# Kernel optimization log

Measured on AMD Instinct MI355X. Metric: run time of the kernel, lower is better.

Reference implementation:

```python
import jax, jax.numpy as jnp
import numpy as np

B, S, HID = 2, 2048, 4096
H, P, N, G, K = 128, 64, 128, 8, 4      # heads, head_dim, ssm_state, groups, conv kernel
INTER = H * P                           # 8192
CONV_DIM = INTER + 2 * G * N            # 10240
CHUNK = 128
EPS = 1e-5
DT_MIN, DT_MAX = 0.0, 100.0


def setup_inputs() -> dict:
    key = jax.random.key(0)
    ks = jax.random.split(key, 4)
    proj = INTER + CONV_DIM + H
    return {
        "x": jax.random.normal(ks[0], (B, S, HID), jnp.float32),
        "in_proj_w": jax.random.normal(ks[1], (proj, HID), jnp.float32) * 0.02,
        "conv_w": jax.random.normal(ks[2], (CONV_DIM, 1, K), jnp.float32) * 0.2,
        "conv_b": jnp.zeros((CONV_DIM,), jnp.float32),
        "dt_bias": jnp.ones((H,), jnp.float32),
        "A_log": jnp.log(jnp.arange(1, H + 1, dtype=jnp.float32)),
        "D": jnp.ones((H,), jnp.float32),
        "norm_w": jnp.ones((INTER,), jnp.float32),
        "out_proj_w": jax.random.normal(ks[3], (HID, INTER), jnp.float32) * 0.02,
    }


def _segsum(a):
    # a: (..., c) -> (..., c, c); [i, j] = sum_{k=j+1..i} a[k] for i >= j, else -inf
    c = a.shape[-1]
    s = jnp.cumsum(a, axis=-1)
    diff = s[..., :, None] - s[..., None, :]
    mask = jnp.tril(jnp.ones((c, c), dtype=bool))
    return jnp.where(mask, diff, -jnp.inf)


def reference(x, in_proj_w, conv_w, conv_b, dt_bias, A_log, D, norm_w, out_proj_w):
    b, s, _ = x.shape
    proj = jnp.einsum('bsd,ed->bse', x, in_proj_w)
    gate = proj[..., :INTER]
    hBC = proj[..., INTER:INTER + CONV_DIM]
    dt = proj[..., INTER + CONV_DIM:]                       # (b, s, H)

    # depthwise causal conv1d + silu
    xc = jnp.transpose(hBC, (0, 2, 1))                      # (b, conv_dim, s)
    xc = jax.lax.conv_general_dilated(xc, conv_w, (1,), [(K - 1, 0)],
                                      dimension_numbers=('NCH', 'OIH', 'NCH'),
                                      feature_group_count=CONV_DIM)
    xc = xc + conv_b[None, :, None]
    hBC = jax.nn.silu(jnp.transpose(xc, (0, 2, 1)))

    hs = hBC[..., :INTER].reshape(b, s, H, P)
    Bm = hBC[..., INTER:INTER + G * N].reshape(b, s, G, N)
    Cm = hBC[..., INTER + G * N:].reshape(b, s, G, N)

    A = -jnp.exp(A_log)                                     # (H,)
    dt = jnp.clip(jax.nn.softplus(dt + dt_bias), DT_MIN, DT_MAX)

    rep = H // G
    Bh = jnp.repeat(Bm, rep, axis=2)                        # (b, s, H, N)
    Ch = jnp.repeat(Cm, rep, axis=2)

    nc = s // CHUNK
    xch = (hs * dt[..., None]).reshape(b, nc, CHUNK, H, P)  # dt-scaled input, chunked
    Bc = Bh.reshape(b, nc, CHUNK, H, N)
    Cc = Ch.reshape(b, nc, CHUNK, H, N)
    A_dt = (dt * A).reshape(b, nc, CHUNK, H).transpose(0, 3, 1, 2)  # (b, H, nc, c)
    A_cum = jnp.cumsum(A_dt, axis=-1)

    # intra-chunk (diagonal) contribution
    L = jnp.exp(_segsum(A_dt))                              # (b, H, nc, c, c)
    Y_diag = jnp.einsum('bzlhn,bzshn,bhzls,bzshp->bzlhp', Cc, Bc, L, xch)

    # per-chunk final states
    decay_states = jnp.exp(A_cum[..., -1:] - A_cum)         # (b, H, nc, c)
    states = jnp.einsum('bzlhn,bhzl,bzlhp->bzhpn', Bc, decay_states, xch)

    # inter-chunk recurrence (initial state = 0)
    states_p = jnp.concatenate([jnp.zeros_like(states[:, :1]), states], axis=1)  # (b, nc+1, H, P, N)
    A_last = jnp.pad(A_cum[..., -1], ((0, 0), (0, 0), (1, 0)))                   # (b, H, nc+1)
    decay_chunk = jnp.exp(_segsum(A_last))                                        # (b, H, nc+1, nc+1)
    new_states = jnp.einsum('bhzc,bchpn->bzhpn', decay_chunk, states_p)
    prev = new_states[:, :-1]                                # state entering each chunk

    Y_off = jnp.einsum('bzlhn,bzhpn,bhzl->bzlhp', Cc, prev, jnp.exp(A_cum))
    Y = (Y_diag + Y_off).reshape(b, s, H, P) + hs * D[None, None, :, None]
    y = Y.reshape(b, s, INTER)

    # gated grouped RMSNorm (norm_before_gate=False)
    g = y * jax.nn.silu(gate)
    gg = g.reshape(b, s, G, INTER // G)
    var = jnp.mean(gg * gg, axis=-1, keepdims=True)
    gg = gg * jax.lax.rsqrt(var + EPS)
    out = gg.reshape(b, s, INTER) * norm_w

    return jnp.einsum('bsi,oi->bso', out, out_proj_w)
```

## Files before the change

### kernel.cpp

```cpp
#include <hip/hip_runtime.h>
#include <hip/hip_bf16.h>
#include <cstdint>
#include <cstddef>

#define DEVI __device__ __forceinline__

#define BB 2
#define S_LEN 2048
#define HID_DIM 4096
#define NH 128
#define PD 64
#define NS 128
#define NG 8
#define INTER 8192
#define CONVD 10240
#define PROJ 18560
#define PROJP 18688
#define NC 16
#define BS 4096
#define GN 1024

using short8 = __attribute__((ext_vector_type(8))) short;
using short4v = __attribute__((ext_vector_type(4))) short;
using f32x4  = __attribute__((ext_vector_type(4))) float;
using bf16x8 = __attribute__((ext_vector_type(8))) __bf16;

DEVI float bf2f(short u) {
  union { unsigned int i; float f; } v;
  v.i = ((unsigned int)(unsigned short)u) << 16;
  return v.f;
}
DEVI short f2bf(float f) {
  union { float ff; unsigned int i; } v; v.ff = f;
  unsigned int x = v.i;
  return (short)((x + 0x7fffu + ((x >> 16) & 1u)) >> 16);
}
DEVI f32x4 mfma16(short8 a, short8 b, f32x4 c) {
  return __builtin_amdgcn_mfma_f32_16x16x32_bf16(
      __builtin_bit_cast(bf16x8, a), __builtin_bit_cast(bf16x8, b), c, 0, 0, 0);
}
DEVI void gl_lds16(const short* g, short* l) {
  __builtin_amdgcn_global_load_lds(
      (const __attribute__((address_space(1))) void*)g,
      (__attribute__((address_space(3))) void*)l, 16, 0, 0);
}
DEVI float sigmoidf_(float x) { return 1.f / (1.f + __expf(-x)); }

__global__ __launch_bounds__(256) void cvt_f32_bf16_k(const float* __restrict__ in,
                                                      short* __restrict__ out, size_t n) {
  size_t i = ((size_t)blockIdx.x * 256 + threadIdx.x) * 8;
  if (i + 8 > n) return;
  float4 a = *(const float4*)(in + i);
  float4 b = *(const float4*)(in + i + 4);
  short8 o;
  o[0] = f2bf(a.x); o[1] = f2bf(a.y); o[2] = f2bf(a.z); o[3] = f2bf(a.w);
  o[4] = f2bf(b.x); o[5] = f2bf(b.y); o[6] = f2bf(b.z); o[7] = f2bf(b.w);
  *(short8*)(out + i) = o;
}


#define STG(ISB, BUF, KH, TILE) do { \
  const short* _src = (ISB) ? Bt : A; \
  const int _r0 = (ISB) ? n0 : m0; \
  short* _lb = lds_ + ((ISB) ? 32768 : 0) + ((BUF)*2+(KH))*8192; \
  const int _kt = (TILE)*64 + (KH)*32; \
  { int _row = (wid*2)*16 + srow; int _sl = sps ^ ((_row>>1)&3); \
    gl_lds16(_src + (size_t)(_r0+_row)*K + _kt + _sl*8, _lb + (wid*2)*512); } \
  { int _row = (wid*2+1)*16 + srow; int _sl = sps ^ ((_row>>1)&3); \
    gl_lds16(_src + (size_t)(_r0+_row)*K + _kt + _sl*8, _lb + (wid*2+1)*512); } \
} while(0)

#define NOPS ((void)0)
#define VM6 asm volatile("s_waitcnt vmcnt(6)" ::: "memory")
#define VM0 asm volatile("s_waitcnt vmcnt(0)" ::: "memory")

#define PH(BUF, KH, MIH, DOB, STGS, VMW) do { \
  _Pragma("unroll") \
  for (int _m = 0; _m < 4; ++_m) { \
    int _row = wr*128 + ((MIH)*4+_m)*16 + fr; \
    af[_m] = *(const short8*)(lds_ + ((BUF)*2+(KH))*8192 + _row*32 + ((slot ^ ((_row>>1)&3))<<3)); \
  } \
  if (DOB) { \
    _Pragma("unroll") \
    for (int _n = 0; _n < 4; ++_n) { \
      int _row = wc*64 + _n*16 + fr; \
      bf_[_n] = *(const short8*)(lds_ + 32768 + ((BUF)*2+(KH))*8192 + _row*32 + ((slot ^ ((_row>>1)&3))<<3)); \
    } \
  } \
  STGS; VMW; \
  __builtin_amdgcn_s_barrier(); \
  asm volatile("s_waitcnt lgkmcnt(0)" ::: "memory"); \
  __builtin_amdgcn_sched_barrier(0); \
  __builtin_amdgcn_s_setprio(1); \
  _Pragma("unroll") \
  for (int _m = 0; _m < 4; ++_m) \
    _Pragma("unroll") \
    for (int _n = 0; _n < 4; ++_n) \
      acc[(MIH)*4+_m][_n] = mfma16(af[_m], bf_[_n], acc[(MIH)*4+_m][_n]); \
  __builtin_amdgcn_s_setprio(0); \
  __builtin_amdgcn_s_barrier(); \
} while(0)

template<int CB16>
__global__ __launch_bounds__(512, 2) void gemm256_k(const short* __restrict__ A,
                                                    const short* __restrict__ Bt,
                                                    void* __restrict__ Cout,
                                                    int Nstride, int K, int ntn) {
  __shared__ short lds_[65536];
  const int tid = threadIdx.x, wid = tid >> 6, lane = tid & 63;
  const int nwg = gridDim.x, orig = blockIdx.x;
  const int swz = (orig & 7) * (nwg >> 3) + (orig >> 3);
  const int per_group = ntn << 4;
  const int group = swz / per_group;
  const int rem = swz - group * per_group;
  const int m0 = (group * 16 + (rem & 15)) * 256;
  const int n0 = (rem >> 4) * 256;
  const int wr = wid >> 2, wc = wid & 3;
  const int fr = lane & 15, slot = lane >> 4;
  const int srow = lane >> 2, sps = lane & 3;

  f32x4 acc[8][4] = {};
  short8 af[4], bf_[4];
  const int NT = K >> 6;

  STG(1, 0, 0, 0); STG(0, 0, 0, 0); STG(1, 0, 1, 0); STG(0, 0, 1, 0);
  asm volatile("s_waitcnt vmcnt(4)" ::: "memory");
  STG(1, 1, 0, 1); STG(0, 1, 0, 1); STG(1, 1, 1, 1);
  asm volatile("s_waitcnt vmcnt(6)" ::: "memory");
  __builtin_amdgcn_s_barrier();

  for (int i = 0; i < (NT >> 1) - 1; ++i) {
    const int t = 2 * i;
    PH(0, 0, 0, 1, STG(0, 1, 1, t + 1), NOPS);
    PH(0, 0, 1, 0, STG(1, 0, 0, t + 2), NOPS);
    PH(0, 1, 0, 1, STG(0, 0, 0, t + 2), NOPS);
    PH(0, 1, 1, 0, STG(1, 0, 1, t + 2), VM6);
    PH(1, 0, 0, 1, STG(0, 0, 1, t + 2), NOPS);
    PH(1, 0, 1, 0, STG(1, 1, 0, t + 3), NOPS);
    PH(1, 1, 0, 1, STG(0, 1, 0, t + 3), NOPS);
    PH(1, 1, 1, 0, STG(1, 1, 1, t + 3), VM6);
  }
  PH(0, 0, 0, 1, STG(0, 1, 1, NT - 1), NOPS);
  PH(0, 0, 1, 0, NOPS, NOPS);
  PH(0, 1, 0, 1, NOPS, NOPS);
  PH(0, 1, 1, 0, NOPS, VM0);
  PH(1, 0, 0, 1, NOPS, NOPS);
  PH(1, 0, 1, 0, NOPS, NOPS);
  PH(1, 1, 0, 1, NOPS, NOPS);
  PH(1, 1, 1, 0, NOPS, NOPS);

  const int er = (lane >> 4) * 4, ec = lane & 15;
  if (CB16) {
    short* C = (short*)Cout;
#pragma unroll
    for (int mi = 0; mi < 8; ++mi)
#pragma unroll
      for (int j = 0; j < 4; ++j) {
        size_t base = (size_t)(m0 + wr * 128 + mi * 16 + er + j) * Nstride + n0 + wc * 64 + ec;
#pragma unroll
        for (int ni = 0; ni < 4; ++ni) C[base + ni * 16] = f2bf(acc[mi][ni][j]);
      }
  } else {
    float* C = (float*)Cout;
#pragma unroll
    for (int mi = 0; mi < 8; ++mi)
#pragma unroll
      for (int j = 0; j < 4; ++j) {
        size_t base = (size_t)(m0 + wr * 128 + mi * 16 + er + j) * Nstride + n0 + wc * 64 + ec;
#pragma unroll
        for (int ni = 0; ni < 4; ++ni) C[base + ni * 16] = acc[mi][ni][j];
      }
  }
}

__global__ __launch_bounds__(256) void conv_silu_k(const short* __restrict__ projb,
                                                   const float* __restrict__ convw,
                                                   const float* __restrict__ convb,
                                                   short* __restrict__ hbc) {
  const int c = blockIdx.x * 256 + threadIdx.x;
  const int s0 = blockIdx.y * 256;
  const int b = blockIdx.z;
  const size_t rb = (size_t)b * S_LEN;
  const float* wp = convw + (size_t)c * 4;
  const float w0 = wp[0], w1 = wp[1], w2 = wp[2], w3 = wp[3];
  const float bias = convb[c];
  const short* pcol = projb + INTER + c;
  float x1 = 0.f, x2 = 0.f, x3 = 0.f;
  if (s0 > 0) {
    x3 = bf2f(pcol[(rb + s0 - 3) * PROJP]);
    x2 = bf2f(pcol[(rb + s0 - 2) * PROJP]);
    x1 = bf2f(pcol[(rb + s0 - 1) * PROJP]);
  }
  for (int s = s0; s < s0 + 256; ++s) {
    float v = bf2f(pcol[(rb + s) * PROJP]);
    float acc = bias + w0 * x3 + w1 * x2 + w2 * x1 + w3 * v;
    float o = acc * sigmoidf_(acc);
    hbc[(rb + s) * CONVD + c] = f2bf(o);
    x3 = x2; x2 = x1; x1 = v;
  }
}

__global__ __launch_bounds__(128) void acum_k(const short* __restrict__ projb,
                                              const float* __restrict__ dt_bias,
                                              const float* __restrict__ A_log,
                                              float* __restrict__ dtT,
                                              float* __restrict__ acum) {
  const int l = threadIdx.x;
  const int z = blockIdx.x, h = blockIdx.y, b = blockIdx.z;
  const float A = -__expf(A_log[h]);
  __shared__ float sv[128];
  const int r = b * S_LEN + z * 128 + l;
  float xv = bf2f(projb[(size_t)r * PROJP + INTER + CONVD + h]) + dt_bias[h];
  float sp = (xv > 20.f) ? xv : log1pf(__expf(xv));
  sp = fminf(fmaxf(sp, 0.f), 100.f);
  const size_t base = ((size_t)(b * NH + h)) * S_LEN + z * 128;
  dtT[base + l] = sp;
  sv[l] = sp * A;
  __syncthreads();
  for (int off = 1; off < 128; off <<= 1) {
    float t = (l >= off) ? sv[l - off] : 0.f;
    __syncthreads();
    sv[l] += t;
    __syncthreads();
  }
  acum[base + l] = sv[l];
}

__global__ __launch_bounds__(512) void states_k(const short* __restrict__ hbc,
                                                const float* __restrict__ dtT,
                                                const float* __restrict__ acum,
                                                float* __restrict__ states) {
  __shared__ short sBT[128 * 128];
  __shared__ short sxdt[64 * 128];
  const int tid = threadIdx.x, wid = tid >> 6, lane = tid & 63;
  const int g = blockIdx.x, z = blockIdx.y, b = blockIdx.z;
  const size_t srow0 = (size_t)(b * S_LEN + z * 128);
  const short* hrow = hbc + srow0 * CONVD;

  {
    const int l = tid & 127, n0b = (tid >> 7) * 32;
    const short* src = hrow + (size_t)l * CONVD + INTER + g * NS + n0b;
    short8 v0 = *(const short8*)(src);
    short8 v1 = *(const short8*)(src + 8);
    short8 v2 = *(const short8*)(src + 16);
    short8 v3 = *(const short8*)(src + 24);
#pragma unroll
    for (int j = 0; j < 8; ++j) {
      sBT[(n0b + j) * 128 + l] = v0[j];
      sBT[(n0b + 8 + j) * 128 + l] = v1[j];
      sBT[(n0b + 16 + j) * 128 + l] = v2[j];
      sBT[(n0b + 24 + j) * 128 + l] = v3[j];
    }
  }

  const int fr = lane & 15, fk8 = (lane >> 4) * 8;
  const int er = (lane >> 4) * 4, ec = lane & 15;
  const int pband = (wid & 3) * 16, nhalf = (wid >> 2) * 64;
  const int s2 = tid & 63, p0w = (tid >> 6) * 8;
  unsigned int* sx32 = (unsigned int*)sxdt;

  for (int hh = 0; hh < 16; ++hh) {
    const int h = g * 16 + hh;
    const float* ac_g = acum + ((size_t)(b * NH + h)) * S_LEN + z * 128;
    const float* dts = dtT + ((size_t)(b * NH + h)) * S_LEN + z * 128;
    __syncthreads();
    {
      const float acL = ac_g[127];
      float dv0 = dts[2 * s2] * __expf(acL - ac_g[2 * s2]);
      float dv1 = dts[2 * s2 + 1] * __expf(acL - ac_g[2 * s2 + 1]);
      const short* rsrc = hrow + (size_t)(2 * s2) * CONVD + (size_t)h * PD + p0w;
      short8 r0 = *(const short8*)(rsrc);
      short8 r1 = *(const short8*)(rsrc + CONVD);
#pragma unroll
      for (int j = 0; j < 8; ++j) {
        unsigned int lo = (unsigned short)f2bf(bf2f(r0[j]) * dv0);
        unsigned int hi = (unsigned short)f2bf(bf2f(r1[j]) * dv1);
        sx32[(p0w + j) * 64 + s2] = lo | (hi << 16);
      }
    }
    __syncthreads();
    f32x4 st[4] = {};
#pragma unroll
    for (int kk = 0; kk < 4; ++kk) {
      short8 a = *(const short8*)(sxdt + (pband + fr) * 128 + kk * 32 + fk8);
#pragma unroll
      for (int ni = 0; ni < 4; ++ni) {
        short8 bb = *(const short8*)(sBT + (nhalf + ni * 16 + fr) * 128 + kk * 32 + fk8);
        st[ni] = mfma16(a, bb, st[ni]);
      }
    }
    float* stp = states + (((size_t)(b * NC + z)) * NH + h) * (size_t)(NS * PD);
#pragma unroll
    for (int ni = 0; ni < 4; ++ni)
#pragma unroll
      for (int j = 0; j < 4; ++j)
        stp[(pband + er + j) * NS + nhalf + ni * 16 + ec] = st[ni][j];
  }
}

__global__ __launch_bounds__(256) void scan_k(float* __restrict__ states,
                                              const float* __restrict__ acum) {
  const int h = blockIdx.x, b = blockIdx.y;
  const int tid = threadIdx.x;
  float* stp = states + ((size_t)(b * NC * NH) + h) * (size_t)(NS * PD);
  const size_t cst = (size_t)NH * NS * PD;
  const float* ac = acum + ((size_t)(b * NH + h)) * S_LEN;
  float E[32];
#pragma unroll
  for (int i = 0; i < 32; ++i) E[i] = 0.f;
  const int n = tid & 127, pg = tid >> 7;
  for (int zz = 0; zz < NC; ++zz) {
    float* sz = stp + (size_t)zz * cst;
    short* pvb = (short*)sz;
    float tmp[32];
#pragma unroll
    for (int i = 0; i < 32; ++i) tmp[i] = sz[i * 256 + tid];
    __syncthreads();
    float dec = __expf(ac[zz * 128 + 127]);
#pragma unroll
    for (int i = 0; i < 32; ++i) {
      int p = i * 2 + pg;
      pvb[p * 128 + n] = f2bf(E[i]);
      E[i] = dec * E[i] + tmp[i];
    }
    __syncthreads();
  }
}

__global__ __launch_bounds__(512) void yfull_k(const short* __restrict__ hbc,
                                               const short* __restrict__ projb,
                                               const float* __restrict__ dtT,
                                               const float* __restrict__ acum,
                                               const float* __restrict__ states,
                                               const float* __restrict__ Dv,
                                               const float* __restrict__ norm_w,
                                               float* __restrict__ Yg,
                                               short* __restrict__ normed) {
  __shared__ short lds[50176];
  __shared__ float sac[128];
  __shared__ float sScale[128];
  __shared__ float sNW[1024];
  short* sC = lds;
  short* sB = lds + 16384;
  short* sxdt = lds + 16384;
  short* sprev = lds + 16384 + 8192;
  const int tid = threadIdx.x, wid = tid >> 6, lane = tid & 63;
  short* sPw = lds + 32768 + wid * 2176;
  const int g = blockIdx.x, z = blockIdx.y, b = blockIdx.z;
  const size_t srow0 = (size_t)(b * S_LEN + z * 128);
  const short* hrow = hbc + srow0 * CONVD;

  {
    const int n0_ = (lane & 15) * 8;
#pragma unroll
    for (int it = 0; it < 4; ++it) {
      int s = it * 32 + wid * 4 + (lane >> 4);
      gl_lds16(hrow + (size_t)s * CONVD + INTER + GN + g * NS + n0_, sC + (it * 32 + wid * 4) * 128);
      gl_lds16(hrow + (size_t)s * CONVD + INTER + g * NS + n0_, sB + (it * 32 + wid * 4) * 128);
    }
  }
  for (int i = tid; i < 1024; i += 512) sNW[i] = norm_w[g * 1024 + i];
  __syncthreads();

  const int fr = lane & 15, fk8 = (lane >> 4) * 8;
  const int er = (lane >> 4) * 4, ec = lane & 15;
  const int lrow = wid * 16;
  const int s2 = tid & 63, p0w = (tid >> 6) * 8;
  unsigned int* sx32 = (unsigned int*)sxdt;

  f32x4 sc[8] = {};
#pragma unroll
  for (int kk = 0; kk < 4; ++kk) {
    short8 a = *(const short8*)(sC + (lrow + fr) * 128 + kk * 32 + fk8);
#pragma unroll
    for (int si = 0; si < 8; ++si) {
      short8 bv = *(const short8*)(sB + (si * 16 + fr) * 128 + kk * 32 + fk8);
      sc[si] = mfma16(a, bv, sc[si]);
    }
  }

  float rssq[4] = {0.f, 0.f, 0.f, 0.f};

  for (int hh = 0; hh < 16; ++hh) {
    const int h = g * 16 + hh;
    const float* ac = acum + ((size_t)(b * NH + h)) * S_LEN + z * 128;
    const float* dts = dtT + ((size_t)(b * NH + h)) * S_LEN + z * 128;
    const short* pvb = (const short*)(states + (((size_t)(b * NC + z)) * NH + h) * (size_t)(NS * PD));
    __syncthreads();
    if (tid < 128) sac[tid] = ac[tid];
    {
      float dv0 = dts[2 * s2], dv1 = dts[2 * s2 + 1];
      const short* rsrc = hrow + (size_t)(2 * s2) * CONVD + (size_t)h * PD + p0w;
      short8 r0 = *(const short8*)(rsrc);
      short8 r1 = *(const short8*)(rsrc + CONVD);
#pragma unroll
      for (int j = 0; j < 8; ++j) {
        unsigned int lo = (unsigned short)f2bf(bf2f(r0[j]) * dv0);
        unsigned int hi = (unsigned short)f2bf(bf2f(r1[j]) * dv1);
        sx32[(p0w + j) * 64 + s2] = lo | (hi << 16);
      }
    }
    gl_lds16(pvb + wid * 1024 + lane * 8, sprev + wid * 1024);
    gl_lds16(pvb + wid * 1024 + 512 + lane * 8, sprev + wid * 1024 + 512);
    __syncthreads();

    {
      float acS[8];
#pragma unroll
      for (int si = 0; si < 8; ++si) acS[si] = sac[si * 16 + ec];
#pragma unroll
      for (int j = 0; j < 4; ++j) {
        int lloc = er + j;
        float acl = sac[lrow + lloc];
#pragma unroll
        for (int si = 0; si < 8; ++si) {
          int s = si * 16 + ec;
          float v = (s <= lrow + lloc) ? sc[si][j] * __expf(acl - acS[si]) : 0.f;
          sPw[lloc * 136 + s] = f2bf(v);
        }
      }
    }
    f32x4 yd[4] = {}, yo[4] = {};
#pragma unroll
    for (int kk = 0; kk < 4; ++kk) {
      short8 ap = *(const short8*)(sPw + fr * 136 + kk * 32 + fk8);
      short8 acf = *(const short8*)(sC + (lrow + fr) * 128 + kk * 32 + fk8);
#pragma unroll
      for (int ni = 0; ni < 4; ++ni) {
        short8 bv = *(const short8*)(sxdt + (ni * 16 + fr) * 128 + kk * 32 + fk8);
        yd[ni] = mfma16(ap, bv, yd[ni]);
        short8 bp = *(const short8*)(sprev + (ni * 16 + fr) * 128 + kk * 32 + fk8);
        yo[ni] = mfma16(acf, bp, yo[ni]);
      }
    }
    const float Dh = Dv[h];
#pragma unroll
    for (int j = 0; j < 4; ++j) {
      int l = lrow + er + j;
      float e_ac = __expf(sac[l]);
#pragma unroll
      for (int ni = 0; ni < 4; ++ni) {
        int p = ni * 16 + ec;
        float hs = bf2f(hrow[(size_t)l * CONVD + (size_t)h * PD + p]);
        float y = yd[ni][j] + yo[ni][j] * e_ac + hs * Dh;
        float gate = bf2f(projb[(srow0 + l) * (size_t)PROJP + (size_t)h * PD + p]);
        float gg = y * gate * sigmoidf_(gate);
        Yg[(srow0 + l) * (size_t)INTER + (size_t)h * PD + p] = gg;
        rssq[j] += gg * gg;
      }
    }
  }

#pragma unroll
  for (int j = 0; j < 4; ++j) {
#pragma unroll
    for (int m = 1; m <= 8; m <<= 1) rssq[j] += __shfl_xor(rssq[j], m, 64);
  }
  if (ec == 0) {
#pragma unroll
    for (int j = 0; j < 4; ++j) sScale[lrow + er + j] = rsqrtf(rssq[j] * (1.f / 1024.f) + 1e-5f);
  }
  __syncthreads();

  for (int e = tid * 8; e < 128 * 1024; e += 4096) {
    int row = e >> 10, ch = e & 1023;
    const float* gp = Yg + (srow0 + row) * (size_t)INTER + g * 1024 + ch;
    float4 g0 = *(const float4*)(gp);
    float4 g1 = *(const float4*)(gp + 4);
    float scl = sScale[row];
    short8 o;
    o[0] = f2bf(g0.x * scl * sNW[ch + 0]); o[1] = f2bf(g0.y * scl * sNW[ch + 1]);
    o[2] = f2bf(g0.z * scl * sNW[ch + 2]); o[3] = f2bf(g0.w * scl * sNW[ch + 3]);
    o[4] = f2bf(g1.x * scl * sNW[ch + 4]); o[5] = f2bf(g1.y * scl * sNW[ch + 5]);
    o[6] = f2bf(g1.z * scl * sNW[ch + 6]); o[7] = f2bf(g1.w * scl * sNW[ch + 7]);
    *(short8*)(normed + (srow0 + row) * (size_t)INTER + g * 1024 + ch) = o;
  }
}

extern "C" void kernel_launch(void* const* d_in, const int* in_sizes, int n_in,
                              void* d_out, int out_size, void* d_ws, size_t ws_size,
                              hipStream_t stream) {
  const float* x     = (const float*)d_in[0];
  const float* w1    = (const float*)d_in[1];
  const float* convw = (const float*)d_in[2];
  const float* convb = (const float*)d_in[3];
  const float* dtb   = (const float*)d_in[4];
  const float* alog  = (const float*)d_in[5];
  const float* Dv    = (const float*)d_in[6];
  const float* nw    = (const float*)d_in[7];
  const float* w2    = (const float*)d_in[8];
  float* out = (float*)d_out;

  char* ws = (char*)d_ws;
  size_t off = 0;
  float* dtT = (float*)(ws + off);  off += (size_t)BB * NH * S_LEN * 4;
  float* acum = (float*)(ws + off); off += (size_t)BB * NH * S_LEN * 4;
  short* xb = (short*)(ws + off);   off += (size_t)BS * HID_DIM * 2;
  char* w1region = ws + off;        off += (size_t)PROJP * HID_DIM * 2;
  short* w1b = (short*)w1region;
  short* normed = (short*)w1region;
  short* w2b = (short*)(w1region + (size_t)BS * INTER * 2);
  short* projb = (short*)(ws + off); off += (size_t)BS * PROJP * 2;
  short* hbc = (short*)(ws + off);   off += (size_t)BS * CONVD * 2;
  float* Y = (float*)(ws + off);     off += (size_t)BS * INTER * 4;
  float* states = (float*)(ws + off); off += (size_t)BB * NC * NH * NS * PD * 4;

  const size_t nx = (size_t)BS * HID_DIM;
  const size_t nw1 = (size_t)PROJ * HID_DIM;
  const size_t nw2 = (size_t)HID_DIM * INTER;

  cvt_f32_bf16_k<<<dim3(nx / 2048), 256, 0, stream>>>(x, xb, nx);
  cvt_f32_bf16_k<<<dim3(nw1 / 2048), 256, 0, stream>>>(w1, w1b, nw1);

  gemm256_k<1><<<dim3(16 * 73), 512, 0, stream>>>(xb, w1b, projb, PROJP, HID_DIM, 73);

  cvt_f32_bf16_k<<<dim3(nw2 / 2048), 256, 0, stream>>>(w2, w2b, nw2);

  conv_silu_k<<<dim3(CONVD / 256, S_LEN / 256, BB), 256, 0, stream>>>(projb, convw, convb, hbc);
  acum_k<<<dim3(NC, NH, BB), 128, 0, stream>>>(projb, dtb, alog, dtT, acum);

  states_k<<<dim3(NG, NC, BB), 512, 0, stream>>>(hbc, dtT, acum, states);
  scan_k<<<dim3(NH, BB), 256, 0, stream>>>(states, acum);
  yfull_k<<<dim3(NG, NC, BB), 512, 0, stream>>>(hbc, projb, dtT, acum, states, Dv, nw, Y, normed);

  gemm256_k<0><<<dim3(16 * 16), 512, 0, stream>>>(normed, w2b, out, HID_DIM, INTER, 16);
}
```

Before: 1.286 ms.

## Double-buffer GEMM LDS fragments, narrow tile swizzle group, store gated Y as bf16

The GEMM main loop now preloads the next phase's A/B fragments from LDS into a second register set while the current MFMAs run, so LDS reads overlap compute instead of waiting before each phase. The workgroup swizzle group shrinks from 16 to 8 M-tiles, which changes L2 reuse. In yfull, the gated intermediate is written as bf16 directly into the normed buffer instead of a separate fp32 buffer, halving that round-trip traffic at a small precision cost. The extra fragment registers may raise register pressure and affect occupancy.

```diff
diff --git a/kernel.cpp b/kernel.cpp
--- a/kernel.cpp
+++ b/kernel.cpp
@@ -74,30 +74,35 @@
 #define VM6 asm volatile("s_waitcnt vmcnt(6)" ::: "memory")
 #define VM0 asm volatile("s_waitcnt vmcnt(0)" ::: "memory")
 
-#define PH(BUF, KH, MIH, DOB, STGS, VMW) do { \
+#define LDAF(DST, BUF, KH, MIH) do { \
   _Pragma("unroll") \
   for (int _m = 0; _m < 4; ++_m) { \
     int _row = wr*128 + ((MIH)*4+_m)*16 + fr; \
-    af[_m] = *(const short8*)(lds_ + ((BUF)*2+(KH))*8192 + _row*32 + ((slot ^ ((_row>>1)&3))<<3)); \
+    DST[_m] = *(const short8*)(lds_ + ((BUF)*2+(KH))*8192 + _row*32 + ((slot ^ ((_row>>1)&3))<<3)); \
   } \
-  if (DOB) { \
-    _Pragma("unroll") \
-    for (int _n = 0; _n < 4; ++_n) { \
-      int _row = wc*64 + _n*16 + fr; \
-      bf_[_n] = *(const short8*)(lds_ + 32768 + ((BUF)*2+(KH))*8192 + _row*32 + ((slot ^ ((_row>>1)&3))<<3)); \
-    } \
+} while(0)
+
+#define LDBF(DST, BUF, KH) do { \
+  _Pragma("unroll") \
+  for (int _n = 0; _n < 4; ++_n) { \
+    int _row = wc*64 + _n*16 + fr; \
+    DST[_n] = *(const short8*)(lds_ + 32768 + ((BUF)*2+(KH))*8192 + _row*32 + ((slot ^ ((_row>>1)&3))<<3)); \
   } \
+} while(0)
+
+#define PH2(CAF, CBF, MIH, PFEN, PFAF, PFBF, PFB, PFKH, PFMIH, PFDOB, STGS, VMW) do { \
   STGS; VMW; \
   __builtin_amdgcn_s_barrier(); \
-  asm volatile("s_waitcnt lgkmcnt(0)" ::: "memory"); \
-  __builtin_amdgcn_sched_barrier(0); \
+  if (PFEN) { LDAF(PFAF, PFB, PFKH, PFMIH); if (PFDOB) LDBF(PFBF, PFB, PFKH); } \
   __builtin_amdgcn_s_setprio(1); \
   _Pragma("unroll") \
   for (int _m = 0; _m < 4; ++_m) \
     _Pragma("unroll") \
     for (int _n = 0; _n < 4; ++_n) \
-      acc[(MIH)*4+_m][_n] = mfma16(af[_m], bf_[_n], acc[(MIH)*4+_m][_n]); \
+      acc[(MIH)*4+_m][_n] = mfma16(CAF[_m], CBF[_n], acc[(MIH)*4+_m][_n]); \
   __builtin_amdgcn_s_setprio(0); \
+  asm volatile("s_waitcnt lgkmcnt(0)" ::: "memory"); \
+  __builtin_amdgcn_sched_barrier(0); \
   __builtin_amdgcn_s_barrier(); \
 } while(0)
 
@@ -110,17 +115,17 @@
   const int tid = threadIdx.x, wid = tid >> 6, lane = tid & 63;
   const int nwg = gridDim.x, orig = blockIdx.x;
   const int swz = (orig & 7) * (nwg >> 3) + (orig >> 3);
-  const int per_group = ntn << 4;
+  const int per_group = ntn << 3;
   const int group = swz / per_group;
   const int rem = swz - group * per_group;
-  const int m0 = (group * 16 + (rem & 15)) * 256;
-  const int n0 = (rem >> 4) * 256;
+  const int m0 = (group * 8 + (rem & 7)) * 256;
+  const int n0 = (rem >> 3) * 256;
   const int wr = wid >> 2, wc = wid & 3;
   const int fr = lane & 15, slot = lane >> 4;
   const int srow = lane >> 2, sps = lane & 3;
 
   f32x4 acc[8][4] = {};
-  short8 af[4], bf_[4];
+  short8 af_a[4], af_b[4], bf_a[4], bf_b[4];
   const int NT = K >> 6;
 
   STG(1, 0, 0, 0); STG(0, 0, 0, 0); STG(1, 0, 1, 0); STG(0, 0, 1, 0);
@@ -128,26 +133,29 @@
   STG(1, 1, 0, 1); STG(0, 1, 0, 1); STG(1, 1, 1, 1);
   asm volatile("s_waitcnt vmcnt(6)" ::: "memory");
   __builtin_amdgcn_s_barrier();
+  LDAF(af_a, 0, 0, 0); LDBF(bf_a, 0, 0);
+  asm volatile("s_waitcnt lgkmcnt(0)" ::: "memory");
+  __builtin_amdgcn_sched_barrier(0);
 
   for (int i = 0; i < (NT >> 1) - 1; ++i) {
     const int t = 2 * i;
-    PH(0, 0, 0, 1, STG(0, 1, 1, t + 1), NOPS);
-    PH(0, 0, 1, 0, STG(1, 0, 0, t + 2), NOPS);
-    PH(0, 1, 0, 1, STG(0, 0, 0, t + 2), NOPS);
-    PH(0, 1, 1, 0, STG(1, 0, 1, t + 2), VM6);
-    PH(1, 0, 0, 1, STG(0, 0, 1, t + 2), NOPS);
-    PH(1, 0, 1, 0, STG(1, 1, 0, t + 3), NOPS);
-    PH(1, 1, 0, 1, STG(0, 1, 0, t + 3), NOPS);
-    PH(1, 1, 1, 0, STG(1, 1, 1, t + 3), VM6);
-  }
-  PH(0, 0, 0, 1, STG(0, 1, 1, NT - 1), NOPS);
-  PH(0, 0, 1, 0, NOPS, NOPS);
-  PH(0, 1, 0, 1, NOPS, NOPS);
-  PH(0, 1, 1, 0, NOPS, VM0);
-  PH(1, 0, 0, 1, NOPS, NOPS);
-  PH(1, 0, 1, 0, NOPS, NOPS);
-  PH(1, 1, 0, 1, NOPS, NOPS);
-  PH(1, 1, 1, 0, NOPS, NOPS);
+    PH2(af_a, bf_a, 0, 1, af_b, bf_a, 0, 0, 1, 0, STG(0, 1, 1, t + 1), NOPS);
+    PH2(af_b, bf_a, 1, 1, af_a, bf_b, 0, 1, 0, 1, STG(1, 0, 0, t + 2), NOPS);
+    PH2(af_a, bf_b, 0, 1, af_b, bf_a, 0, 1, 1, 0, STG(0, 0, 0, t + 2), NOPS);
+    PH2(af_b, bf_b, 1, 1, af_a, bf_a, 1, 0, 0, 1, STG(1, 0, 1, t + 2), VM6);
+    PH2(af_a, bf_a, 0, 1, af_b, bf_b, 1, 0, 1, 0, STG(0, 0, 1, t + 2), NOPS);
+    PH2(af_b, bf_a, 1, 1, af_a, bf_b, 1, 1, 0, 1, STG(1, 1, 0, t + 3), NOPS);
+    PH2(af_a, bf_b, 0, 1, af_b, bf_a, 1, 1, 1, 0, STG(0, 1, 0, t + 3), NOPS);
+    PH2(af_b, bf_b, 1, 1, af_a, bf_a, 0, 0, 0, 1, STG(1, 1, 1, t + 3), VM6);
+  }
+  PH2(af_a, bf_a, 0, 1, af_b, bf_a, 0, 0, 1, 0, STG(0, 1, 1, NT - 1), NOPS);
+  PH2(af_b, bf_a, 1, 1, af_a, bf_b, 0, 1, 0, 1, NOPS, NOPS);
+  PH2(af_a, bf_b, 0, 1, af_b, bf_a, 0, 1, 1, 0, NOPS, NOPS);
+  PH2(af_b, bf_b, 1, 1, af_a, bf_a, 1, 0, 0, 1, NOPS, VM0);
+  PH2(af_a, bf_a, 0, 1, af_b, bf_b, 1, 0, 1, 0, NOPS, NOPS);
+  PH2(af_b, bf_a, 1, 1, af_a, bf_b, 1, 1, 0, 1, NOPS, NOPS);
+  PH2(af_a, bf_b, 0, 1, af_b, bf_a, 1, 1, 1, 0, NOPS, NOPS);
+  PH2(af_b, bf_b, 1, 0, af_a, bf_a, 0, 0, 0, 0, NOPS, NOPS);
 
   const int er = (lane >> 4) * 4, ec = lane & 15;
   if (CB16) {
@@ -334,7 +342,6 @@
                                                const float* __restrict__ states,
                                                const float* __restrict__ Dv,
                                                const float* __restrict__ norm_w,
-                                               float* __restrict__ Yg,
                                                short* __restrict__ normed) {
   __shared__ short lds[50176];
   __shared__ float sac[128];
@@ -445,7 +452,7 @@
         float y = yd[ni][j] + yo[ni][j] * e_ac + hs * Dh;
         float gate = bf2f(projb[(srow0 + l) * (size_t)PROJP + (size_t)h * PD + p]);
         float gg = y * gate * sigmoidf_(gate);
-        Yg[(srow0 + l) * (size_t)INTER + (size_t)h * PD + p] = gg;
+        normed[(srow0 + l) * (size_t)INTER + (size_t)h * PD + p] = f2bf(gg);
         rssq[j] += gg * gg;
       }
     }
@@ -464,16 +471,13 @@
 
   for (int e = tid * 8; e < 128 * 1024; e += 4096) {
     int row = e >> 10, ch = e & 1023;
-    const float* gp = Yg + (srow0 + row) * (size_t)INTER + g * 1024 + ch;
-    float4 g0 = *(const float4*)(gp);
-    float4 g1 = *(const float4*)(gp + 4);
+    short* gp = normed + (srow0 + row) * (size_t)INTER + g * 1024 + ch;
+    short8 gv = *(const short8*)(gp);
     float scl = sScale[row];
     short8 o;
-    o[0] = f2bf(g0.x * scl * sNW[ch + 0]); o[1] = f2bf(g0.y * scl * sNW[ch + 1]);
-    o[2] = f2bf(g0.z * scl * sNW[ch + 2]); o[3] = f2bf(g0.w * scl * sNW[ch + 3]);
-    o[4] = f2bf(g1.x * scl * sNW[ch + 4]); o[5] = f2bf(g1.y * scl * sNW[ch + 5]);
-    o[6] = f2bf(g1.z * scl * sNW[ch + 6]); o[7] = f2bf(g1.w * scl * sNW[ch + 7]);
-    *(short8*)(normed + (srow0 + row) * (size_t)INTER + g * 1024 + ch) = o;
+#pragma unroll
+    for (int q = 0; q < 8; ++q) o[q] = f2bf(bf2f(gv[q]) * scl * sNW[ch + q]);
+    *(short8*)(gp) = o;
   }
 }
 
@@ -502,7 +506,6 @@
   short* w2b = (short*)(w1region + (size_t)BS * INTER * 2);
   short* projb = (short*)(ws + off); off += (size_t)BS * PROJP * 2;
   short* hbc = (short*)(ws + off);   off += (size_t)BS * CONVD * 2;
-  float* Y = (float*)(ws + off);     off += (size_t)BS * INTER * 4;
   float* states = (float*)(ws + off); off += (size_t)BB * NC * NH * NS * PD * 4;
 
   const size_t nx = (size_t)BS * HID_DIM;
@@ -521,7 +524,7 @@
 
   states_k<<<dim3(NG, NC, BB), 512, 0, stream>>>(hbc, dtT, acum, states);
   scan_k<<<dim3(NH, BB), 256, 0, stream>>>(states, acum);
-  yfull_k<<<dim3(NG, NC, BB), 512, 0, stream>>>(hbc, projb, dtT, acum, states, Dv, nw, Y, normed);
+  yfull_k<<<dim3(NG, NC, BB), 512, 0, stream>>>(hbc, projb, dtT, acum, states, Dv, nw, normed);
 
   gemm256_k<0><<<dim3(16 * 16), 512, 0, stream>>>(normed, w2b, out, HID_DIM, INTER, 16);
 }
```

Result: faster. 1.250 ms (-2.8%).
